# Kernel optimization log

Hardware: AMD Instinct MI355X
Metric: run time of the kernel (lower is better)

The kernel has to match this reference:

```python
import jax, jax.numpy as jnp
import numpy as np

B, H, S, D = 4, 16, 2048, 64

def setup_inputs() -> dict:
    key = jax.random.key(0)
    k1, k2, k3 = jax.random.split(key, 3)
    Q = jax.random.normal(k1, (B, H, S, D), dtype=jnp.float32)
    K = jax.random.normal(k2, (B, H, S, D), dtype=jnp.float32)
    V = jax.random.normal(k3, (B, H, S, D), dtype=jnp.float32)
    # causal boolean mask, broadcast over batch/heads
    mask = jnp.tril(jnp.ones((S, S), dtype=bool))
    return {"Q": Q, "K": K, "V": V, "mask": mask}

def reference(Q, K, V, mask):
    d_k = Q.shape[-1]
    # [..., m, n] score matrix
    qk = jnp.einsum('...md,...nd->...mn', Q, K) / jnp.sqrt(jnp.float32(d_k))
    neg_inf = jnp.float32(-jnp.inf)
    scores = qk + jnp.where(mask, jnp.float32(0.0), neg_inf)
    # numerically stable softmax over last dim (matches SoftmaxModule)
    probs = jax.nn.softmax(scores, axis=-1)
    return jnp.einsum('...mn,...nd->...md', probs, V)
```

## Files before the change

### kernel.cpp

```cpp
#include <hip/hip_runtime.h>

#define S_LEN 2048
#define D_DIM 64
#define BM    128
#define BN    64
#define NW    4
#define NT    (NW * 64)
#define BH    64
#define QB    (S_LEN / BM)

typedef __attribute__((ext_vector_type(4)))  _Float16 half4;
typedef __attribute__((ext_vector_type(8)))  _Float16 half8;
typedef __attribute__((ext_vector_type(16))) float    f32x16;

#define MFMA3216(a, b, c) __builtin_amdgcn_mfma_f32_32x32x16_f16((a), (b), (c), 0, 0, 0)


__global__ __launch_bounds__(NT, 4) void fa_fwd(const float* __restrict__ Q,
                                                const float* __restrict__ K,
                                                const float* __restrict__ V,
                                                float* __restrict__ Out) {
  __shared__ _Float16 kh[2][BN][68];
  __shared__ _Float16 vT[2][D_DIM][68];

  const int tid  = threadIdx.x;
  const int wave = tid >> 6;
  const int lane = tid & 63;
  const int h    = lane >> 5;
  const int qc   = lane & 31;

  const int bid = blockIdx.x;
  const int c   = bid & 255;
  const int g   = bid >> 8;
  const int a   = c >> 6;
  const int bh  = c & 63;
  const int qb  = (g & 1) ? (2 * (g - 1) + a) : (15 - 2 * g - a);
  const int q0  = qb * BM;
  const int q0w = q0 + wave * 32;
  const long base = (long)bh * S_LEN * D_DIM;

  const float SCALE = 0.125f * 1.44269504088896340736f;

  half8 qf[4];
  {
    const float* qp = Q + base + (long)(q0w + qc) * D_DIM;
#pragma unroll
    for (int cc = 0; cc < 4; ++cc) {
      float4 u = *(const float4*)(qp + 16 * cc + 8 * h);
      float4 v = *(const float4*)(qp + 16 * cc + 8 * h + 4);
      half8 t;
      t[0] = (_Float16)(u.x * SCALE); t[1] = (_Float16)(u.y * SCALE);
      t[2] = (_Float16)(u.z * SCALE); t[3] = (_Float16)(u.w * SCALE);
      t[4] = (_Float16)(v.x * SCALE); t[5] = (_Float16)(v.y * SCALE);
      t[6] = (_Float16)(v.z * SCALE); t[7] = (_Float16)(v.w * SCALE);
      qf[cc] = t;
    }
  }

  f32x16 o0, o1;
#pragma unroll
  for (int e = 0; e < 16; ++e) { o0[e] = 0.f; o1[e] = 0.f; }
  float l = 0.f;

  const int nTiles = (q0 + BM) / BN;
  const int myEnd  = q0w + 31;

  const int skey = tid >> 2, sc = (tid & 3) * 16;
  const int sd   = tid & 63, sr = tid >> 6;
  const float* kstage = K + base + (long)skey * D_DIM + sc;
  const float* vstage = V + base + (long)(16 * sr) * D_DIM + sd;

  union H8 { half4 q[2]; half8 o; };

  float kreg[16], vreg[16];

  {
#pragma unroll
    for (int j = 0; j < 4; ++j)
      *(float4*)&kreg[4 * j] = *(const float4*)(kstage + 4 * j);
#pragma unroll
    for (int j = 0; j < 16; ++j) vreg[j] = vstage[(long)j * D_DIM];
#pragma unroll
    for (int j = 0; j < 4; ++j) {
      half4 t;
      t[0] = (_Float16)kreg[4 * j];     t[1] = (_Float16)kreg[4 * j + 1];
      t[2] = (_Float16)kreg[4 * j + 2]; t[3] = (_Float16)kreg[4 * j + 3];
      *(half4*)&kh[0][skey][sc + 4 * j] = t;
    }
#pragma unroll
    for (int p = 0; p < 4; ++p) {
      constexpr int inv[4] = {0, 2, 1, 3};
      half4 t;
#pragma unroll
      for (int j = 0; j < 4; ++j) t[j] = (_Float16)vreg[inv[p] * 4 + j];
      *(half4*)&vT[0][sd][16 * sr + 4 * p] = t;
    }
  }
  __syncthreads();

  for (int t = 0; t < nTiles; ++t) {
    const int n0   = t * BN;
    const int cur  = t & 1;
    const bool more = (t + 1 < nTiles);

    if (more) {
      const float* kp = kstage + (long)(t + 1) * BN * D_DIM;
      const float* vp = vstage + (long)(t + 1) * BN * D_DIM;
#pragma unroll
      for (int j = 0; j < 4; ++j)
        *(float4*)&kreg[4 * j] = *(const float4*)(kp + 4 * j);
#pragma unroll
      for (int j = 0; j < 16; ++j) vreg[j] = vp[(long)j * D_DIM];
    }

    if (n0 <= myEnd) {
      const _Float16 (*khc)[68] = kh[cur];
      const _Float16 (*vTc)[68] = vT[cur];
#pragma unroll
      for (int s = 0; s < 2; ++s) {
        const int sbase = n0 + 32 * s;
        if (sbase > myEnd) break;

        f32x16 st;
#pragma unroll
        for (int e = 0; e < 16; ++e) st[e] = 0.f;
#pragma unroll
        for (int cc = 0; cc < 4; ++cc) {
          H8 kf;
          kf.q[0] = *(const half4*)&khc[32 * s + qc][16 * cc + 8 * h];
          kf.q[1] = *(const half4*)&khc[32 * s + qc][16 * cc + 8 * h + 4];
          st = MFMA3216(kf.o, qf[cc], st);
        }

        if (sbase + 31 > q0w) {
#pragma unroll
          for (int e = 0; e < 16; ++e) {
            int key = sbase + (e & 3) + 8 * (e >> 2) + 4 * h;
            if (key > q0w + qc) st[e] = -1e30f;
          }
        }

#pragma unroll
        for (int e = 0; e < 16; ++e) st[e] = __builtin_amdgcn_exp2f(st[e]);
        {
          float t0 = (st[0] + st[1])   + (st[2] + st[3]);
          float t1 = (st[4] + st[5])   + (st[6] + st[7]);
          float t2 = (st[8] + st[9])   + (st[10] + st[11]);
          float t3 = (st[12] + st[13]) + (st[14] + st[15]);
          l += (t0 + t1) + (t2 + t3);
        }

#pragma unroll
        for (int cl = 0; cl < 2; ++cl) {
          half8 pf;
#pragma unroll
          for (int j = 0; j < 8; ++j) pf[j] = (_Float16)st[8 * cl + j];
          const int cg = 2 * s + cl;
          H8 v0, v1;
          v0.q[0] = *(const half4*)&vTc[qc][16 * cg + 8 * h];
          v0.q[1] = *(const half4*)&vTc[qc][16 * cg + 8 * h + 4];
          v1.q[0] = *(const half4*)&vTc[32 + qc][16 * cg + 8 * h];
          v1.q[1] = *(const half4*)&vTc[32 + qc][16 * cg + 8 * h + 4];
          o0 = MFMA3216(v0.o, pf, o0);
          o1 = MFMA3216(v1.o, pf, o1);
        }
      }
    }

    if (more) {
      const int nb = cur ^ 1;
#pragma unroll
      for (int j = 0; j < 4; ++j) {
        half4 t2;
        t2[0] = (_Float16)kreg[4 * j];     t2[1] = (_Float16)kreg[4 * j + 1];
        t2[2] = (_Float16)kreg[4 * j + 2]; t2[3] = (_Float16)kreg[4 * j + 3];
        *(half4*)&kh[nb][skey][sc + 4 * j] = t2;
      }
#pragma unroll
      for (int p = 0; p < 4; ++p) {
        constexpr int inv[4] = {0, 2, 1, 3};
        half4 t2;
#pragma unroll
        for (int j = 0; j < 4; ++j) t2[j] = (_Float16)vreg[inv[p] * 4 + j];
        *(half4*)&vT[nb][sd][16 * sr + 4 * p] = t2;
      }
    }
    __syncthreads();
  }

  l += __shfl_xor(l, 32);
  const float invl = 1.0f / l;
  float* op = Out + base + (long)(q0w + qc) * D_DIM;
#pragma unroll
  for (int e = 0; e < 16; ++e) {
    int d = (e & 3) + 8 * (e >> 2) + 4 * h;
    op[d]      = o0[e] * invl;
    op[32 + d] = o1[e] * invl;
  }
}

extern "C" void kernel_launch(void* const* d_in, const int* in_sizes, int n_in,
                              void* d_out, int out_size, void* d_ws, size_t ws_size,
                              hipStream_t stream) {
  const float* Q = (const float*)d_in[0];
  const float* K = (const float*)d_in[1];
  const float* V = (const float*)d_in[2];
  (void)in_sizes; (void)n_in; (void)d_ws; (void)ws_size; (void)out_size;
  float* Out = (float*)d_out;
  dim3 grid(BH * QB);
  dim3 block(NT);
  hipLaunchKernelGGL(fa_fwd, grid, block, 0, stream, Q, K, V, Out);
}
```

Measured before the change: 179.1 us.

## Split block into compute and producer warp groups for K/V staging

Doubles the block to 512 threads. The first four waves only compute attention from shared memory, and four new waves load K/V from global memory, convert them to half and write the next buffer. This is meant to take global-load latency and conversion work off the compute waves' critical path. It doubles the threads per block and relies on matching __syncthreads counts across the divergent branches. It also changes launch bounds to (512, 8), which may force heavy register limits and cause spills.

```diff
diff --git a/kernel.cpp b/kernel.cpp
--- a/kernel.cpp
+++ b/kernel.cpp
@@ -4,8 +4,7 @@
 #define D_DIM 64
 #define BM    128
 #define BN    64
-#define NW    4
-#define NT    (NW * 64)
+#define NT    512
 #define BH    64
 #define QB    (S_LEN / BM)
 
@@ -16,18 +15,14 @@
 #define MFMA3216(a, b, c) __builtin_amdgcn_mfma_f32_32x32x16_f16((a), (b), (c), 0, 0, 0)
 
 
-__global__ __launch_bounds__(NT, 4) void fa_fwd(const float* __restrict__ Q,
+__global__ __launch_bounds__(NT, 8) void fa_fwd(const float* __restrict__ Q,
                                                 const float* __restrict__ K,
                                                 const float* __restrict__ V,
                                                 float* __restrict__ Out) {
   __shared__ _Float16 kh[2][BN][68];
   __shared__ _Float16 vT[2][D_DIM][68];
 
-  const int tid  = threadIdx.x;
-  const int wave = tid >> 6;
-  const int lane = tid & 63;
-  const int h    = lane >> 5;
-  const int qc   = lane & 31;
+  const int tid = threadIdx.x;
 
   const int bid = blockIdx.x;
   const int c   = bid & 255;
@@ -36,166 +31,164 @@
   const int bh  = c & 63;
   const int qb  = (g & 1) ? (2 * (g - 1) + a) : (15 - 2 * g - a);
   const int q0  = qb * BM;
-  const int q0w = q0 + wave * 32;
   const long base = (long)bh * S_LEN * D_DIM;
+  const int nTiles = 2 * (qb + 1);
 
   const float SCALE = 0.125f * 1.44269504088896340736f;
 
-  half8 qf[4];
-  {
-    const float* qp = Q + base + (long)(q0w + qc) * D_DIM;
-#pragma unroll
-    for (int cc = 0; cc < 4; ++cc) {
-      float4 u = *(const float4*)(qp + 16 * cc + 8 * h);
-      float4 v = *(const float4*)(qp + 16 * cc + 8 * h + 4);
-      half8 t;
-      t[0] = (_Float16)(u.x * SCALE); t[1] = (_Float16)(u.y * SCALE);
-      t[2] = (_Float16)(u.z * SCALE); t[3] = (_Float16)(u.w * SCALE);
-      t[4] = (_Float16)(v.x * SCALE); t[5] = (_Float16)(v.y * SCALE);
-      t[6] = (_Float16)(v.z * SCALE); t[7] = (_Float16)(v.w * SCALE);
-      qf[cc] = t;
-    }
-  }
-
-  f32x16 o0, o1;
-#pragma unroll
-  for (int e = 0; e < 16; ++e) { o0[e] = 0.f; o1[e] = 0.f; }
-  float l = 0.f;
-
-  const int nTiles = (q0 + BM) / BN;
-  const int myEnd  = q0w + 31;
-
-  const int skey = tid >> 2, sc = (tid & 3) * 16;
-  const int sd   = tid & 63, sr = tid >> 6;
-  const float* kstage = K + base + (long)skey * D_DIM + sc;
-  const float* vstage = V + base + (long)(16 * sr) * D_DIM + sd;
-
   union H8 { half4 q[2]; half8 o; };
 
-  float kreg[16], vreg[16];
-
-  {
-#pragma unroll
-    for (int j = 0; j < 4; ++j)
-      *(float4*)&kreg[4 * j] = *(const float4*)(kstage + 4 * j);
-#pragma unroll
-    for (int j = 0; j < 16; ++j) vreg[j] = vstage[(long)j * D_DIM];
-#pragma unroll
-    for (int j = 0; j < 4; ++j) {
-      half4 t;
-      t[0] = (_Float16)kreg[4 * j];     t[1] = (_Float16)kreg[4 * j + 1];
-      t[2] = (_Float16)kreg[4 * j + 2]; t[3] = (_Float16)kreg[4 * j + 3];
-      *(half4*)&kh[0][skey][sc + 4 * j] = t;
-    }
-#pragma unroll
-    for (int p = 0; p < 4; ++p) {
-      constexpr int inv[4] = {0, 2, 1, 3};
-      half4 t;
-#pragma unroll
-      for (int j = 0; j < 4; ++j) t[j] = (_Float16)vreg[inv[p] * 4 + j];
-      *(half4*)&vT[0][sd][16 * sr + 4 * p] = t;
-    }
-  }
-  __syncthreads();
-
-  for (int t = 0; t < nTiles; ++t) {
-    const int n0   = t * BN;
-    const int cur  = t & 1;
-    const bool more = (t + 1 < nTiles);
-
-    if (more) {
-      const float* kp = kstage + (long)(t + 1) * BN * D_DIM;
-      const float* vp = vstage + (long)(t + 1) * BN * D_DIM;
-#pragma unroll
-      for (int j = 0; j < 4; ++j)
-        *(float4*)&kreg[4 * j] = *(const float4*)(kp + 4 * j);
-#pragma unroll
-      for (int j = 0; j < 16; ++j) vreg[j] = vp[(long)j * D_DIM];
-    }
-
-    if (n0 <= myEnd) {
-      const _Float16 (*khc)[68] = kh[cur];
-      const _Float16 (*vTc)[68] = vT[cur];
-#pragma unroll
-      for (int s = 0; s < 2; ++s) {
-        const int sbase = n0 + 32 * s;
-        if (sbase > myEnd) break;
-
-        f32x16 st;
-#pragma unroll
-        for (int e = 0; e < 16; ++e) st[e] = 0.f;
-#pragma unroll
-        for (int cc = 0; cc < 4; ++cc) {
-          H8 kf;
-          kf.q[0] = *(const half4*)&khc[32 * s + qc][16 * cc + 8 * h];
-          kf.q[1] = *(const half4*)&khc[32 * s + qc][16 * cc + 8 * h + 4];
-          st = MFMA3216(kf.o, qf[cc], st);
-        }
-
-        if (sbase + 31 > q0w) {
-#pragma unroll
-          for (int e = 0; e < 16; ++e) {
-            int key = sbase + (e & 3) + 8 * (e >> 2) + 4 * h;
-            if (key > q0w + qc) st[e] = -1e30f;
-          }
-        }
-
-#pragma unroll
-        for (int e = 0; e < 16; ++e) st[e] = __builtin_amdgcn_exp2f(st[e]);
-        {
-          float t0 = (st[0] + st[1])   + (st[2] + st[3]);
-          float t1 = (st[4] + st[5])   + (st[6] + st[7]);
-          float t2 = (st[8] + st[9])   + (st[10] + st[11]);
-          float t3 = (st[12] + st[13]) + (st[14] + st[15]);
-          l += (t0 + t1) + (t2 + t3);
-        }
-
-#pragma unroll
-        for (int cl = 0; cl < 2; ++cl) {
-          half8 pf;
-#pragma unroll
-          for (int j = 0; j < 8; ++j) pf[j] = (_Float16)st[8 * cl + j];
-          const int cg = 2 * s + cl;
-          H8 v0, v1;
-          v0.q[0] = *(const half4*)&vTc[qc][16 * cg + 8 * h];
-          v0.q[1] = *(const half4*)&vTc[qc][16 * cg + 8 * h + 4];
-          v1.q[0] = *(const half4*)&vTc[32 + qc][16 * cg + 8 * h];
-          v1.q[1] = *(const half4*)&vTc[32 + qc][16 * cg + 8 * h + 4];
-          o0 = MFMA3216(v0.o, pf, o0);
-          o1 = MFMA3216(v1.o, pf, o1);
+  if (tid < 256) {
+    const int wave = tid >> 6;
+    const int lane = tid & 63;
+    const int h    = lane >> 5;
+    const int qc   = lane & 31;
+    const int q0w  = q0 + wave * 32;
+    const int myEnd = q0w + 31;
+
+    half8 qf[4];
+    {
+      const float* qp = Q + base + (long)(q0w + qc) * D_DIM;
+#pragma unroll
+      for (int cc = 0; cc < 4; ++cc) {
+        float4 u = *(const float4*)(qp + 16 * cc + 8 * h);
+        float4 v = *(const float4*)(qp + 16 * cc + 8 * h + 4);
+        half8 t;
+        t[0] = (_Float16)(u.x * SCALE); t[1] = (_Float16)(u.y * SCALE);
+        t[2] = (_Float16)(u.z * SCALE); t[3] = (_Float16)(u.w * SCALE);
+        t[4] = (_Float16)(v.x * SCALE); t[5] = (_Float16)(v.y * SCALE);
+        t[6] = (_Float16)(v.z * SCALE); t[7] = (_Float16)(v.w * SCALE);
+        qf[cc] = t;
+      }
+    }
+
+    f32x16 o0, o1;
+#pragma unroll
+    for (int e = 0; e < 16; ++e) { o0[e] = 0.f; o1[e] = 0.f; }
+    float l = 0.f;
+
+    __syncthreads();
+
+    for (int t = 0; t < nTiles; ++t) {
+      const int n0  = t * BN;
+      const int cur = t & 1;
+      if (n0 <= myEnd) {
+        const _Float16 (*khc)[68] = kh[cur];
+        const _Float16 (*vTc)[68] = vT[cur];
+#pragma unroll
+        for (int s = 0; s < 2; ++s) {
+          const int sbase = n0 + 32 * s;
+          if (sbase > myEnd) break;
+
+          f32x16 st;
+#pragma unroll
+          for (int e = 0; e < 16; ++e) st[e] = 0.f;
+#pragma unroll
+          for (int cc = 0; cc < 4; ++cc) {
+            H8 kf;
+            kf.q[0] = *(const half4*)&khc[32 * s + qc][16 * cc + 8 * h];
+            kf.q[1] = *(const half4*)&khc[32 * s + qc][16 * cc + 8 * h + 4];
+            st = MFMA3216(kf.o, qf[cc], st);
+          }
+
+          if (sbase + 31 > q0w) {
+#pragma unroll
+            for (int e = 0; e < 16; ++e) {
+              int key = sbase + (e & 3) + 8 * (e >> 2) + 4 * h;
+              if (key > q0w + qc) st[e] = -1e30f;
+            }
+          }
+
+#pragma unroll
+          for (int e = 0; e < 16; ++e) st[e] = __builtin_amdgcn_exp2f(st[e]);
+          {
+            float t0 = (st[0] + st[1])   + (st[2] + st[3]);
+            float t1 = (st[4] + st[5])   + (st[6] + st[7]);
+            float t2 = (st[8] + st[9])   + (st[10] + st[11]);
+            float t3 = (st[12] + st[13]) + (st[14] + st[15]);
+            l += (t0 + t1) + (t2 + t3);
+          }
+
+#pragma unroll
+          for (int cl = 0; cl < 2; ++cl) {
+            half8 pf;
+#pragma unroll
+            for (int j = 0; j < 8; ++j) pf[j] = (_Float16)st[8 * cl + j];
+            const int cg = 2 * s + cl;
+            H8 v0, v1;
+            v0.q[0] = *(const half4*)&vTc[qc][16 * cg + 8 * h];
+            v0.q[1] = *(const half4*)&vTc[qc][16 * cg + 8 * h + 4];
+            v1.q[0] = *(const half4*)&vTc[32 + qc][16 * cg + 8 * h];
+            v1.q[1] = *(const half4*)&vTc[32 + qc][16 * cg + 8 * h + 4];
+            o0 = MFMA3216(v0.o, pf, o0);
+            o1 = MFMA3216(v1.o, pf, o1);
+          }
         }
       }
-    }
-
-    if (more) {
-      const int nb = cur ^ 1;
-#pragma unroll
-      for (int j = 0; j < 4; ++j) {
-        half4 t2;
-        t2[0] = (_Float16)kreg[4 * j];     t2[1] = (_Float16)kreg[4 * j + 1];
-        t2[2] = (_Float16)kreg[4 * j + 2]; t2[3] = (_Float16)kreg[4 * j + 3];
-        *(half4*)&kh[nb][skey][sc + 4 * j] = t2;
+      __syncthreads();
+    }
+
+    l += __shfl_xor(l, 32);
+    const float invl = 1.0f / l;
+    float* op = Out + base + (long)(q0w + qc) * D_DIM;
+#pragma unroll
+    for (int e = 0; e < 16; ++e) {
+      int d = (e & 3) + 8 * (e >> 2) + 4 * h;
+      op[d]      = o0[e] * invl;
+      op[32 + d] = o1[e] * invl;
+    }
+  } else {
+    const int ptid = tid - 256;
+    const int skey = ptid >> 2, sc = (ptid & 3) * 16;
+    const int sd   = ptid & 63, sr = ptid >> 6;
+    const float* kstage = K + base + (long)skey * D_DIM + sc;
+    const float* vstage = V + base + (long)(16 * sr) * D_DIM + sd;
+
+    float kreg[16], vreg[16];
+
+#define PLOAD(T)                                                             \
+    {                                                                        \
+      const float* kp = kstage + (long)(T) * BN * D_DIM;                     \
+      const float* vp = vstage + (long)(T) * BN * D_DIM;                     \
+      _Pragma("unroll")                                                      \
+      for (int j = 0; j < 4; ++j)                                            \
+        *(float4*)&kreg[4 * j] = *(const float4*)(kp + 4 * j);               \
+      _Pragma("unroll")                                                      \
+      for (int j = 0; j < 16; ++j) vreg[j] = vp[(long)j * D_DIM];            \
+    }
+
+#define PWRITE(B)                                                            \
+    {                                                                        \
+      _Pragma("unroll")                                                      \
+      for (int j = 0; j < 4; ++j) {                                          \
+        half4 tk;                                                            \
+        tk[0] = (_Float16)kreg[4 * j];     tk[1] = (_Float16)kreg[4 * j + 1];\
+        tk[2] = (_Float16)kreg[4 * j + 2]; tk[3] = (_Float16)kreg[4 * j + 3];\
+        *(half4*)&kh[B][skey][sc + 4 * j] = tk;                              \
+      }                                                                      \
+      _Pragma("unroll")                                                      \
+      for (int p = 0; p < 4; ++p) {                                          \
+        constexpr int inv[4] = {0, 2, 1, 3};         \
+        half4 tv4;                                                           \
+        _Pragma("unroll")                                                    \
+        for (int j = 0; j < 4; ++j) tv4[j] = (_Float16)vreg[inv[p] * 4 + j]; \
+        *(half4*)&vT[B][sd][16 * sr + 4 * p] = tv4;                          \
+      }                                                                      \
+    }
+
+    PLOAD(0);
+    PWRITE(0);
+    __syncthreads();
+
+    for (int t = 0; t < nTiles; ++t) {
+      if (t + 1 < nTiles) {
+        PLOAD(t + 1);
+        PWRITE((t + 1) & 1);
       }
-#pragma unroll
-      for (int p = 0; p < 4; ++p) {
-        constexpr int inv[4] = {0, 2, 1, 3};
-        half4 t2;
-#pragma unroll
-        for (int j = 0; j < 4; ++j) t2[j] = (_Float16)vreg[inv[p] * 4 + j];
-        *(half4*)&vT[nb][sd][16 * sr + 4 * p] = t2;
-      }
-    }
-    __syncthreads();
-  }
-
-  l += __shfl_xor(l, 32);
-  const float invl = 1.0f / l;
-  float* op = Out + base + (long)(q0w + qc) * D_DIM;
-#pragma unroll
-  for (int e = 0; e < 16; ++e) {
-    int d = (e & 3) + 8 * (e >> 2) + 4 * h;
-    op[d]      = o0[e] * invl;
-    op[32 + d] = o1[e] * invl;
+      __syncthreads();
+    }
+#undef PLOAD
+#undef PWRITE
   }
 }
 
```

Result: slower. 560.9 us (+213.1%).

## Split long causal query blocks across two workgroups with atomic-counter merge

Applied to the files above, without the earlier changes.

Query blocks 8-15, which have the most key tiles under the causal mask, are split into two halves of the key range, giving 24 work items per head instead of 16 so the work is spread more evenly. Each half writes unnormalised partial outputs and row sums to the output or to workspace. An atomic counter lets the second finisher combine the halves and normalise. This adds a memset launch, extra global traffic and fences, and only runs when the workspace is large enough.

```diff
diff --git a/kernel.cpp b/kernel.cpp
--- a/kernel.cpp
+++ b/kernel.cpp
@@ -9,6 +9,12 @@
 #define BH    64
 #define QB    (S_LEN / BM)
 
+#define NSPLIT        512
+#define WS_OB_FLOATS  (NSPLIT * 128 * 64)
+#define WS_L_FLOATS   (NSPLIT * 256)
+#define WS_CNT_OFF    ((WS_OB_FLOATS + WS_L_FLOATS) * 4)
+#define WS_NEED       (WS_CNT_OFF + NSPLIT * 4)
+
 typedef __attribute__((ext_vector_type(4)))  _Float16 half4;
 typedef __attribute__((ext_vector_type(8)))  _Float16 half8;
 typedef __attribute__((ext_vector_type(16))) float    f32x16;
@@ -16,12 +22,30 @@
 #define MFMA3216(a, b, c) __builtin_amdgcn_mfma_f32_32x32x16_f16((a), (b), (c), 0, 0, 0)
 
 
+static __device__ const signed char ITEM_QB[24] =
+  {15,15, 7,14,14,13,13, 6,12,12,11,11, 5,10,10, 9, 9, 4, 8, 8, 3, 2, 1, 0};
+static __device__ const signed char ITEM_T0[24] =
+  { 0,16, 0, 0,15, 0,14, 0, 0,13, 0,12, 0, 0,11, 0,10, 0, 0, 9, 0, 0, 0, 0};
+static __device__ const signed char ITEM_T1[24] =
+  {16,32,16,15,30,14,28,14,13,26,12,24,12,11,22,10,20,10, 9,18, 8, 6, 4, 2};
+
+static __device__ __forceinline__ void ast(float* p, float v) {
+  __hip_atomic_store(p, v, __ATOMIC_RELAXED, __HIP_MEMORY_SCOPE_AGENT);
+}
+static __device__ __forceinline__ float ald(const float* p) {
+  return __hip_atomic_load(p, __ATOMIC_RELAXED, __HIP_MEMORY_SCOPE_AGENT);
+}
+
+template <bool SPLIT>
 __global__ __launch_bounds__(NT, 4) void fa_fwd(const float* __restrict__ Q,
                                                 const float* __restrict__ K,
                                                 const float* __restrict__ V,
-                                                float* __restrict__ Out) {
+                                                float* __restrict__ Out,
+                                                float* __restrict__ wsF,
+                                                int* __restrict__ wsCnt) {
   __shared__ _Float16 kh[2][BN][68];
   __shared__ _Float16 vT[2][D_DIM][68];
+  __shared__ int lastFlag;
 
   const int tid  = threadIdx.x;
   const int wave = tid >> 6;
@@ -29,12 +53,21 @@
   const int h    = lane >> 5;
   const int qc   = lane & 31;
 
-  const int bid = blockIdx.x;
-  const int c   = bid & 255;
-  const int g   = bid >> 8;
-  const int a   = c >> 6;
-  const int bh  = c & 63;
-  const int qb  = (g & 1) ? (2 * (g - 1) + a) : (15 - 2 * g - a);
+  int bh, qb, t0, t1, sid = 0;
+  bool isSplit = false, halfB = false;
+  if constexpr (SPLIT) {
+    const int item = blockIdx.x >> 6;
+    bh = blockIdx.x & 63;
+    qb = ITEM_QB[item]; t0 = ITEM_T0[item]; t1 = ITEM_T1[item];
+    isSplit = (qb >= 8);
+    halfB   = (t0 != 0);
+    sid     = (qb - 8) * 64 + bh;
+  } else {
+    const int c = blockIdx.x & 255, g = blockIdx.x >> 8, a = c >> 6;
+    bh = c & 63;
+    qb = (g & 1) ? (2 * (g - 1) + a) : (15 - 2 * g - a);
+    t0 = 0; t1 = 2 * (qb + 1);
+  }
   const int q0  = qb * BM;
   const int q0w = q0 + wave * 32;
   const long base = (long)bh * S_LEN * D_DIM;
@@ -62,8 +95,7 @@
   for (int e = 0; e < 16; ++e) { o0[e] = 0.f; o1[e] = 0.f; }
   float l = 0.f;
 
-  const int nTiles = (q0 + BM) / BN;
-  const int myEnd  = q0w + 31;
+  const int myEnd = q0w + 31;
 
   const int skey = tid >> 2, sc = (tid & 3) * 16;
   const int sd   = tid & 63, sr = tid >> 6;
@@ -75,17 +107,20 @@
   float kreg[16], vreg[16];
 
   {
+    const float* kp = kstage + (long)t0 * BN * D_DIM;
+    const float* vp = vstage + (long)t0 * BN * D_DIM;
 #pragma unroll
     for (int j = 0; j < 4; ++j)
-      *(float4*)&kreg[4 * j] = *(const float4*)(kstage + 4 * j);
-#pragma unroll
-    for (int j = 0; j < 16; ++j) vreg[j] = vstage[(long)j * D_DIM];
+      *(float4*)&kreg[4 * j] = *(const float4*)(kp + 4 * j);
+#pragma unroll
+    for (int j = 0; j < 16; ++j) vreg[j] = vp[(long)j * D_DIM];
+    const int b0 = t0 & 1;
 #pragma unroll
     for (int j = 0; j < 4; ++j) {
       half4 t;
       t[0] = (_Float16)kreg[4 * j];     t[1] = (_Float16)kreg[4 * j + 1];
       t[2] = (_Float16)kreg[4 * j + 2]; t[3] = (_Float16)kreg[4 * j + 3];
-      *(half4*)&kh[0][skey][sc + 4 * j] = t;
+      *(half4*)&kh[b0][skey][sc + 4 * j] = t;
     }
 #pragma unroll
     for (int p = 0; p < 4; ++p) {
@@ -93,15 +128,15 @@
       half4 t;
 #pragma unroll
       for (int j = 0; j < 4; ++j) t[j] = (_Float16)vreg[inv[p] * 4 + j];
-      *(half4*)&vT[0][sd][16 * sr + 4 * p] = t;
+      *(half4*)&vT[b0][sd][16 * sr + 4 * p] = t;
     }
   }
   __syncthreads();
 
-  for (int t = 0; t < nTiles; ++t) {
+  for (int t = t0; t < t1; ++t) {
     const int n0   = t * BN;
     const int cur  = t & 1;
-    const bool more = (t + 1 < nTiles);
+    const bool more = (t + 1 < t1);
 
     if (more) {
       const float* kp = kstage + (long)(t + 1) * BN * D_DIM;
@@ -143,11 +178,11 @@
 #pragma unroll
         for (int e = 0; e < 16; ++e) st[e] = __builtin_amdgcn_exp2f(st[e]);
         {
-          float t0 = (st[0] + st[1])   + (st[2] + st[3]);
-          float t1 = (st[4] + st[5])   + (st[6] + st[7]);
-          float t2 = (st[8] + st[9])   + (st[10] + st[11]);
-          float t3 = (st[12] + st[13]) + (st[14] + st[15]);
-          l += (t0 + t1) + (t2 + t3);
+          float u0 = (st[0] + st[1])   + (st[2] + st[3]);
+          float u1 = (st[4] + st[5])   + (st[6] + st[7]);
+          float u2 = (st[8] + st[9])   + (st[10] + st[11]);
+          float u3 = (st[12] + st[13]) + (st[14] + st[15]);
+          l += (u0 + u1) + (u2 + u3);
         }
 
 #pragma unroll
@@ -168,7 +203,7 @@
     }
 
     if (more) {
-      const int nb = cur ^ 1;
+      const int nb = (t + 1) & 1;
 #pragma unroll
       for (int j = 0; j < 4; ++j) {
         half4 t2;
@@ -189,13 +224,50 @@
   }
 
   l += __shfl_xor(l, 32);
-  const float invl = 1.0f / l;
-  float* op = Out + base + (long)(q0w + qc) * D_DIM;
-#pragma unroll
-  for (int e = 0; e < 16; ++e) {
-    int d = (e & 3) + 8 * (e >> 2) + 4 * h;
-    op[d]      = o0[e] * invl;
-    op[32 + d] = o1[e] * invl;
+
+  if (!isSplit) {
+    const float invl = 1.0f / l;
+    float* op = Out + base + (long)(q0w + qc) * D_DIM;
+#pragma unroll
+    for (int e = 0; e < 16; ++e) {
+      int d = (e & 3) + 8 * (e >> 2) + 4 * h;
+      op[d]      = o0[e] * invl;
+      op[32 + d] = o1[e] * invl;
+    }
+  } else {
+    const int lrow = wave * 32 + qc;
+    float* obase = halfB ? (wsF + (long)sid * 8192)
+                         : (Out + base + (long)q0 * D_DIM);
+    float* lbase = wsF + WS_OB_FLOATS + (long)sid * 256 + (halfB ? 128 : 0);
+#pragma unroll
+    for (int e = 0; e < 16; ++e) {
+      int d = (e & 3) + 8 * (e >> 2) + 4 * h;
+      ast(&obase[(long)lrow * 64 + d],      o0[e]);
+      ast(&obase[(long)lrow * 64 + d + 32], o1[e]);
+    }
+    if (h == 0) ast(&lbase[lrow], l);
+    __threadfence();
+    __syncthreads();
+    if (tid == 0) {
+      lastFlag = __hip_atomic_fetch_add(&wsCnt[sid], 1, __ATOMIC_ACQ_REL,
+                                        __HIP_MEMORY_SCOPE_AGENT);
+    }
+    __syncthreads();
+    if (lastFlag == 1) {
+      float* op = Out + base + (long)q0 * D_DIM;
+      const float* ob = wsF + (long)sid * 8192;
+      const float* lb = wsF + WS_OB_FLOATS + (long)sid * 256;
+      const float lT  = ald(&lb[lrow]) + ald(&lb[128 + lrow]);
+      const float invl = 1.0f / lT;
+#pragma unroll
+      for (int e = 0; e < 16; ++e) {
+        int d = (e & 3) + 8 * (e >> 2) + 4 * h;
+        long i0 = (long)lrow * 64 + d;
+        long i1 = i0 + 32;
+        op[i0] = (ald(&op[i0]) + ald(&ob[i0])) * invl;
+        op[i1] = (ald(&op[i1]) + ald(&ob[i1])) * invl;
+      }
+    }
   }
 }
 
@@ -205,9 +277,16 @@
   const float* Q = (const float*)d_in[0];
   const float* K = (const float*)d_in[1];
   const float* V = (const float*)d_in[2];
-  (void)in_sizes; (void)n_in; (void)d_ws; (void)ws_size; (void)out_size;
+  (void)in_sizes; (void)n_in; (void)out_size;
   float* Out = (float*)d_out;
-  dim3 grid(BH * QB);
-  dim3 block(NT);
-  hipLaunchKernelGGL(fa_fwd, grid, block, 0, stream, Q, K, V, Out);
-}
+  if (d_ws != nullptr && ws_size >= (size_t)WS_NEED) {
+    float* wsF  = (float*)d_ws;
+    int*   wsCnt = (int*)((char*)d_ws + WS_CNT_OFF);
+    hipMemsetAsync(wsCnt, 0, NSPLIT * 4, stream);
+    hipLaunchKernelGGL(HIP_KERNEL_NAME(fa_fwd<true>), dim3(24 * BH), dim3(NT),
+                       0, stream, Q, K, V, Out, wsF, wsCnt);
+  } else {
+    hipLaunchKernelGGL(HIP_KERNEL_NAME(fa_fwd<false>), dim3(BH * QB), dim3(NT),
+                       0, stream, Q, K, V, Out, (float*)d_ws, (int*)d_ws);
+  }
+}
```

After: 544.1 us. +203.7%, slower.
